# Performance work log

Hardware: AMD Instinct MI355X
Metric: run time of the kernel (lower is better)

## Reference

```python
import jax, jax.numpy as jnp
import numpy as np

VOCAB, HIDDEN, EMB_DIM = 30522, 768, 128
B, QLEN, DLEN = 1024, 32, 180
NEG = -1e4  # masked doc-token similarity
EPS = 1e-12


def setup_inputs() -> dict:
    key = jax.random.key(0)
    k1, k2, k3, k4, k5, k6 = jax.random.split(key, 6)
    return {
        "query_input_ids": jax.random.randint(k1, (B, QLEN), 0, VOCAB, dtype=jnp.int64) if jax.config.jax_enable_x64 else jax.random.randint(k1, (B, QLEN), 0, VOCAB, dtype=jnp.int32),
        "query_attention_mask": jax.random.randint(k2, (B, QLEN), 0, 2, dtype=jnp.int32),
        "doc_input_ids": jax.random.randint(k3, (B, DLEN), 0, VOCAB, dtype=jnp.int32),
        "doc_attention_mask": jax.random.randint(k4, (B, DLEN), 0, 2, dtype=jnp.int32),
        "embed_table": jax.random.normal(k5, (VOCAB, HIDDEN), dtype=jnp.float32) * 0.02,
        "proj_w": jax.random.normal(k6, (HIDDEN, EMB_DIM), dtype=jnp.float32) * 0.02,
        "proj_b": jnp.zeros((EMB_DIM,), dtype=jnp.float32),
    }


def _encode(ids, embed_table, proj_w, proj_b):
    # token embedding lookup -> linear projection -> L2 normalize (ColBERT-style)
    h = embed_table[ids]                      # (B, L, HIDDEN)
    e = jnp.einsum('blh,hd->bld', h, proj_w) + proj_b  # (B, L, EMB_DIM)
    e = e / (jnp.linalg.norm(e, axis=-1, keepdims=True) + EPS)
    return e


def reference(query_input_ids, query_attention_mask, doc_input_ids,
              doc_attention_mask, embed_table, proj_w, proj_b):
    q = _encode(query_input_ids, embed_table, proj_w, proj_b)  # (B, Q, D)
    d = _encode(doc_input_ids, embed_table, proj_w, proj_b)    # (B, T, D)
    # Batched MaxSim: sim[b,q,t] = <q_emb, d_emb>
    sim = jnp.einsum('bqd,btd->bqt', q, d)
    sim = jnp.where(doc_attention_mask[:, None, :] > 0, sim, NEG)
    max_sim = sim.max(axis=-1)                                  # (B, Q)
    scores = (max_sim * query_attention_mask.astype(max_sim.dtype)).sum(axis=-1)
    return scores  # (B,)
```

## Files before the change

kernel.cpp:

```cpp
#include <hip/hip_runtime.h>
#include <math.h>

#define VOCAB  30522
#define HIDDEN 768
#define EMB    128
#define BATCH  1024
#define QLEN   32
#define DLEN   180
#define NEGV   (-1e4f)

typedef __attribute__((ext_vector_type(8))) short bf16x8;
typedef __attribute__((ext_vector_type(4))) float f32x4;
typedef unsigned int u32;

__device__ __forceinline__ unsigned short f2bf(float x) {
  union { float f; unsigned u; } v; v.f = x;
  unsigned r = v.u + 0x7FFFu + ((v.u >> 16) & 1u);
  return (unsigned short)(r >> 16);
}
__device__ __forceinline__ float bf2f(unsigned short h) {
  union { float f; unsigned u; } v; v.u = ((unsigned)h) << 16;
  return v.f;
}
__device__ __forceinline__ void split_pk(float x0, float x1, unsigned& h, unsigned& l) {
  asm("v_cvt_pk_bf16_f32 %0, %1, %2" : "=v"(h) : "v"(x0), "v"(x1));
  float h0, h1;
  h0 = __uint_as_float(h << 16);
  h1 = __uint_as_float(h & 0xffff0000u);
  float l0 = x0 - h0, l1 = x1 - h1;
  asm("v_cvt_pk_bf16_f32 %0, %1, %2" : "=v"(l) : "v"(l0), "v"(l1));
}
__device__ __forceinline__ void gload16(const float* g, void* l) {
  __builtin_amdgcn_global_load_lds(
      (const __attribute__((address_space(1))) u32*)g,
      (__attribute__((address_space(3))) u32*)l, 16, 0, 0);
}

__global__ __launch_bounds__(256) void prep_wfrag(
    const float* __restrict__ W, unsigned short* __restrict__ wfh,
    unsigned short* __restrict__ wfl) {
  int g = blockIdx.x * 256 + threadIdx.x;
  if (g >= 24 * 8 * 64) return;
  int lane = g & 63, nt = (g >> 6) & 7, kk = g >> 9;
  int lr = lane & 15, kq = lane >> 4;
  int n = nt * 16 + lr;
  int k0 = kk * 32 + kq * 8;
  unsigned short hh[8], ll[8];
#pragma unroll
  for (int j = 0; j < 8; ++j) {
    float x = W[(size_t)(k0 + j) * EMB + n];
    unsigned short hi = f2bf(x);
    hh[j] = hi;
    ll[j] = f2bf(x - bf2f(hi));
  }
  size_t base = (size_t)g * 8;
#pragma unroll
  for (int j = 0; j < 2; ++j) {
    *(ushort4*)(wfh + base + j * 4) = *(ushort4*)(hh + j * 4);
    *(ushort4*)(wfl + base + j * 4) = *(ushort4*)(ll + j * 4);
  }
}

__global__ __launch_bounds__(256) void colbert_proj_mfma(
    const float* __restrict__ emb, const unsigned short* __restrict__ wfh,
    const unsigned short* __restrict__ wfl, const float* __restrict__ bias,
    unsigned short* __restrict__ pebf) {
  __shared__ __align__(16) char smem[17408];

  const int tid  = threadIdx.x;
  const int lane = tid & 63;
  const int wid  = tid >> 6;
  const int lr   = lane & 15;
  const int kq   = lane >> 4;
  const int row0 = blockIdx.x * 32;

#define GSRC(P, HC)                                                            \
  (emb + (size_t)(row0 + ((P) >> 4) > VOCAB - 1 ? VOCAB - 1                    \
                                                : row0 + ((P) >> 4)) * HIDDEN  \
       + (HC) * 64 + (((P) & 15) ^ (((P) >> 4) & 7)) * 4)

#define GLOAD(HC, BUF)                                                         \
  {                                                                            \
    char* d = smem + (BUF) * 8192;                                             \
    gload16(GSRC(tid, HC),       d + tid * 16);                                \
    gload16(GSRC(tid + 256, HC), d + 4096 + tid * 16);                         \
  }

  f32x4 acc[2][2];
#pragma unroll
  for (int mi = 0; mi < 2; ++mi)
#pragma unroll
    for (int ni = 0; ni < 2; ++ni) acc[mi][ni] = (f32x4)0.f;

  GLOAD(0, 0);
  __syncthreads();

  for (int hc = 0; hc < 12; ++hc) {
    const int cur = hc & 1;
    if (hc < 11) GLOAD(hc + 1, cur ^ 1);
    bf16x8 bh[2][2], bl[2][2];
#pragma unroll
    for (int kk = 0; kk < 2; ++kk)
#pragma unroll
      for (int ni = 0; ni < 2; ++ni) {
        size_t g = ((size_t)((hc * 2 + kk) * 8 + wid * 2 + ni) * 64 + lane) * 8;
        bh[kk][ni] = *(const bf16x8*)(wfh + g);
        bl[kk][ni] = *(const bf16x8*)(wfl + g);
      }
    char* Ab = smem + cur * 8192;
#pragma unroll
    for (int kk = 0; kk < 2; ++kk) {
      bf16x8 ah[2], al[2];
#pragma unroll
      for (int mi = 0; mi < 2; ++mi) {
        int row = mi * 16 + lr;
        int base = row * 256 + kk * 128 + kq * 32;
        float4 x0 = *(float4*)(Ab + ((base)      ^ ((row & 7) << 4)));
        float4 x1 = *(float4*)(Ab + ((base + 16) ^ ((row & 7) << 4)));
        union { unsigned u[4]; bf16x8 v; } H, L;
        split_pk(x0.x, x0.y, H.u[0], L.u[0]);
        split_pk(x0.z, x0.w, H.u[1], L.u[1]);
        split_pk(x1.x, x1.y, H.u[2], L.u[2]);
        split_pk(x1.z, x1.w, H.u[3], L.u[3]);
        ah[mi] = H.v; al[mi] = L.v;
      }
#pragma unroll
      for (int mi = 0; mi < 2; ++mi)
#pragma unroll
        for (int ni = 0; ni < 2; ++ni) {
          acc[mi][ni] = __builtin_amdgcn_mfma_f32_16x16x32_bf16(ah[mi], bh[kk][ni], acc[mi][ni], 0, 0, 0);
          acc[mi][ni] = __builtin_amdgcn_mfma_f32_16x16x32_bf16(ah[mi], bl[kk][ni], acc[mi][ni], 0, 0, 0);
          acc[mi][ni] = __builtin_amdgcn_mfma_f32_16x16x32_bf16(al[mi], bh[kk][ni], acc[mi][ni], 0, 0, 0);
        }
    }
    __syncthreads();
  }

  float* ep = (float*)smem;
#pragma unroll
  for (int ni = 0; ni < 2; ++ni) {
    int col = wid * 32 + ni * 16 + lr;
    float bb = bias[col];
#pragma unroll
    for (int mi = 0; mi < 2; ++mi)
#pragma unroll
      for (int j = 0; j < 4; ++j) {
        int r = mi * 16 + kq * 4 + j;
        ep[r * 132 + col] = acc[mi][ni][j] + bb;
      }
  }
  __syncthreads();
  {
    int row = tid >> 3, oct = tid & 7;
    float4 vv[4];
    float ss = 0.f;
#pragma unroll
    for (int i = 0; i < 4; ++i) {
      vv[i] = *(float4*)&ep[row * 132 + oct * 16 + i * 4];
      ss += vv[i].x * vv[i].x + vv[i].y * vv[i].y + vv[i].z * vv[i].z + vv[i].w * vv[i].w;
    }
    ss += __shfl_xor(ss, 1);
    ss += __shfl_xor(ss, 2);
    ss += __shfl_xor(ss, 4);
    float sc = 1.f / (sqrtf(ss) + 1e-12f);
    int gr = row0 + row;
    if (gr < VOCAB) {
      unsigned pk[8];
#pragma unroll
      for (int i = 0; i < 4; ++i) {
        pk[i * 2 + 0] = (unsigned)f2bf(vv[i].x * sc) | ((unsigned)f2bf(vv[i].y * sc) << 16);
        pk[i * 2 + 1] = (unsigned)f2bf(vv[i].z * sc) | ((unsigned)f2bf(vv[i].w * sc) << 16);
      }
      uint4* dst = (uint4*)(pebf + (size_t)gr * EMB + oct * 16);
      dst[0] = make_uint4(pk[0], pk[1], pk[2], pk[3]);
      dst[1] = make_uint4(pk[4], pk[5], pk[6], pk[7]);
    }
  }
#undef GSRC
#undef GLOAD
}

__global__ __launch_bounds__(256) void colbert_score_mfma(
    const int* __restrict__ qids, const int* __restrict__ qmask,
    const int* __restrict__ dids, const int* __restrict__ dmask,
    const unsigned short* __restrict__ pebf, float* __restrict__ out) {
  __shared__ int sqid[32];
  __shared__ int sdid[192];
  __shared__ unsigned char smsk[192];
  __shared__ float wmax[4][32];

  const int b    = blockIdx.x;
  const int tid  = threadIdx.x;
  const int lane = tid & 63;
  const int wid  = tid >> 6;
  const int lr   = lane & 15;
  const int kq   = lane >> 4;

  if (tid < 32) sqid[tid] = qids[b * QLEN + tid];
  if (tid < 192) {
    if (tid < DLEN) {
      sdid[tid] = dids[b * DLEN + tid];
      smsk[tid] = (unsigned char)(dmask[b * DLEN + tid] > 0 ? 1 : 0);
    } else {
      sdid[tid] = 0;
      smsk[tid] = 0;
    }
  }
  __syncthreads();

  bf16x8 af[2][4];
#pragma unroll
  for (int mi = 0; mi < 2; ++mi) {
    size_t base = (size_t)sqid[mi * 16 + lr] * EMB + kq * 8;
#pragma unroll
    for (int ks = 0; ks < 4; ++ks)
      af[mi][ks] = *(const bf16x8*)(pebf + base + ks * 32);
  }
  const int n0 = wid * 48;
  bf16x8 bfr[3][4];
#pragma unroll
  for (int ni = 0; ni < 3; ++ni) {
    size_t base = (size_t)sdid[n0 + ni * 16 + lr] * EMB + kq * 8;
#pragma unroll
    for (int ks = 0; ks < 4; ++ks)
      bfr[ni][ks] = *(const bf16x8*)(pebf + base + ks * 32);
  }

  f32x4 acc[2][3];
#pragma unroll
  for (int mi = 0; mi < 2; ++mi)
#pragma unroll
    for (int ni = 0; ni < 3; ++ni) acc[mi][ni] = (f32x4)0.f;

#pragma unroll
  for (int ks = 0; ks < 4; ++ks)
#pragma unroll
    for (int mi = 0; mi < 2; ++mi)
#pragma unroll
      for (int ni = 0; ni < 3; ++ni)
        acc[mi][ni] = __builtin_amdgcn_mfma_f32_16x16x32_bf16(af[mi][ks], bfr[ni][ks], acc[mi][ni], 0, 0, 0);

#pragma unroll
  for (int mi = 0; mi < 2; ++mi) {
#pragma unroll
    for (int j = 0; j < 4; ++j) {
      float m = -3.0e38f;
#pragma unroll
      for (int ni = 0; ni < 3; ++ni) {
        int t = n0 + ni * 16 + lr;
        float s = smsk[t] ? acc[mi][ni][j] : NEGV;
        m = fmaxf(m, s);
      }
#pragma unroll
      for (int x = 1; x < 16; x <<= 1) m = fmaxf(m, __shfl_xor(m, x));
      if (lr == 0) wmax[wid][mi * 16 + kq * 4 + j] = m;
    }
  }
  __syncthreads();

  if (tid < 32) {
    float m = fmaxf(fmaxf(wmax[0][tid], wmax[1][tid]),
                    fmaxf(wmax[2][tid], wmax[3][tid]));
    float s = m * (float)qmask[b * QLEN + tid];
#pragma unroll
    for (int x = 1; x < 32; x <<= 1) s += __shfl_xor(s, x);
    if (tid == 0) out[b] = s;
  }
}

extern "C" void kernel_launch(void* const* d_in, const int* in_sizes, int n_in,
                              void* d_out, int out_size, void* d_ws, size_t ws_size,
                              hipStream_t stream) {
  const int*   qids  = (const int*)d_in[0];
  const int*   qmask = (const int*)d_in[1];
  const int*   dids  = (const int*)d_in[2];
  const int*   dmask = (const int*)d_in[3];
  const float* emb   = (const float*)d_in[4];
  const float* W     = (const float*)d_in[5];
  const float* bias  = (const float*)d_in[6];
  float*       out   = (float*)d_out;

  char* ws = (char*)d_ws;
  unsigned short* pebf = (unsigned short*)ws;
  unsigned short* wfh  = (unsigned short*)(ws + 7813632);
  unsigned short* wfl  = (unsigned short*)(ws + 7813632 + 196608);

  prep_wfrag<<<48, 256, 0, stream>>>(W, wfh, wfl);
  colbert_proj_mfma<<<(VOCAB + 31) / 32, 256, 0, stream>>>(emb, wfh, wfl, bias, pebf);
  colbert_score_mfma<<<BATCH, 256, 0, stream>>>(qids, qmask, dids, dmask, pebf, out);
}
```

Before: 51.94 us.

## Shrink projection tile to 16 rows and preload full row slab into LDS

The vocabulary projection kernel now processes 16 embedding rows per block instead of 32, which doubles the grid size to raise parallelism across CUs. It replaces the double-buffered 64-column chunk pipeline with one upfront load of the whole 16x768 fp32 slab into 48KB of LDS, removing the per-iteration barriers. The trade-off is that each block re-reads the W fragments for half as many rows, doubling total W traffic, and the larger LDS footprint may limit how many blocks fit on a CU.

```diff
diff --git a/kernel.cpp b/kernel.cpp
--- a/kernel.cpp
+++ b/kernel.cpp
@@ -65,39 +65,31 @@
     const float* __restrict__ emb, const unsigned short* __restrict__ wfh,
     const unsigned short* __restrict__ wfl, const float* __restrict__ bias,
     unsigned short* __restrict__ pebf) {
-  __shared__ __align__(16) char smem[17408];
+  __shared__ __align__(16) char smem[49152];
 
   const int tid  = threadIdx.x;
   const int lane = tid & 63;
   const int wid  = tid >> 6;
   const int lr   = lane & 15;
   const int kq   = lane >> 4;
-  const int row0 = blockIdx.x * 32;
-
-#define GSRC(P, HC)                                                            \
-  (emb + (size_t)(row0 + ((P) >> 4) > VOCAB - 1 ? VOCAB - 1                    \
-                                                : row0 + ((P) >> 4)) * HIDDEN  \
-       + (HC) * 64 + (((P) & 15) ^ (((P) >> 4) & 7)) * 4)
-
-#define GLOAD(HC, BUF)                                                         \
-  {                                                                            \
-    char* d = smem + (BUF) * 8192;                                             \
-    gload16(GSRC(tid, HC),       d + tid * 16);                                \
-    gload16(GSRC(tid + 256, HC), d + 4096 + tid * 16);                         \
-  }
-
-  f32x4 acc[2][2];
-#pragma unroll
-  for (int mi = 0; mi < 2; ++mi)
-#pragma unroll
-    for (int ni = 0; ni < 2; ++ni) acc[mi][ni] = (f32x4)0.f;
-
-  GLOAD(0, 0);
-  __syncthreads();
+  const int row0 = blockIdx.x * 16;
+
+  {
+    int srow = tid >> 4;
+    int gr = row0 + srow; if (gr > VOCAB - 1) gr = VOCAB - 1;
+    const float* rowp = emb + (size_t)gr * HIDDEN
+                        + (size_t)(((tid & 15) ^ (srow & 7)) * 4);
+#pragma unroll
+    for (int i = 0; i < 12; ++i) {
+      gload16(rowp + i * 64, smem + i * 4096 + tid * 16);
+    }
+  }
+  __syncthreads();
+
+  f32x4 acc[2];
+  acc[0] = (f32x4)0.f; acc[1] = (f32x4)0.f;
 
   for (int hc = 0; hc < 12; ++hc) {
-    const int cur = hc & 1;
-    if (hc < 11) GLOAD(hc + 1, cur ^ 1);
     bf16x8 bh[2][2], bl[2][2];
 #pragma unroll
     for (int kk = 0; kk < 2; ++kk)
@@ -107,77 +99,59 @@
         bh[kk][ni] = *(const bf16x8*)(wfh + g);
         bl[kk][ni] = *(const bf16x8*)(wfl + g);
       }
-    char* Ab = smem + cur * 8192;
+    char* Ab = smem + hc * 4096;
 #pragma unroll
     for (int kk = 0; kk < 2; ++kk) {
-      bf16x8 ah[2], al[2];
-#pragma unroll
-      for (int mi = 0; mi < 2; ++mi) {
-        int row = mi * 16 + lr;
-        int base = row * 256 + kk * 128 + kq * 32;
-        float4 x0 = *(float4*)(Ab + ((base)      ^ ((row & 7) << 4)));
-        float4 x1 = *(float4*)(Ab + ((base + 16) ^ ((row & 7) << 4)));
-        union { unsigned u[4]; bf16x8 v; } H, L;
-        split_pk(x0.x, x0.y, H.u[0], L.u[0]);
-        split_pk(x0.z, x0.w, H.u[1], L.u[1]);
-        split_pk(x1.x, x1.y, H.u[2], L.u[2]);
-        split_pk(x1.z, x1.w, H.u[3], L.u[3]);
-        ah[mi] = H.v; al[mi] = L.v;
+      int s0 = kk * 8 + kq * 2;
+      float4 x0 = *(float4*)(Ab + lr * 256 + ((s0)     ^ (lr & 7)) * 16);
+      float4 x1 = *(float4*)(Ab + lr * 256 + ((s0 + 1) ^ (lr & 7)) * 16);
+      union { unsigned u[4]; bf16x8 v; } H, L;
+      split_pk(x0.x, x0.y, H.u[0], L.u[0]);
+      split_pk(x0.z, x0.w, H.u[1], L.u[1]);
+      split_pk(x1.x, x1.y, H.u[2], L.u[2]);
+      split_pk(x1.z, x1.w, H.u[3], L.u[3]);
+#pragma unroll
+      for (int ni = 0; ni < 2; ++ni) {
+        acc[ni] = __builtin_amdgcn_mfma_f32_16x16x32_bf16(H.v, bh[kk][ni], acc[ni], 0, 0, 0);
+        acc[ni] = __builtin_amdgcn_mfma_f32_16x16x32_bf16(H.v, bl[kk][ni], acc[ni], 0, 0, 0);
+        acc[ni] = __builtin_amdgcn_mfma_f32_16x16x32_bf16(L.v, bh[kk][ni], acc[ni], 0, 0, 0);
       }
-#pragma unroll
-      for (int mi = 0; mi < 2; ++mi)
-#pragma unroll
-        for (int ni = 0; ni < 2; ++ni) {
-          acc[mi][ni] = __builtin_amdgcn_mfma_f32_16x16x32_bf16(ah[mi], bh[kk][ni], acc[mi][ni], 0, 0, 0);
-          acc[mi][ni] = __builtin_amdgcn_mfma_f32_16x16x32_bf16(ah[mi], bl[kk][ni], acc[mi][ni], 0, 0, 0);
-          acc[mi][ni] = __builtin_amdgcn_mfma_f32_16x16x32_bf16(al[mi], bh[kk][ni], acc[mi][ni], 0, 0, 0);
-        }
-    }
-    __syncthreads();
-  }
-
+    }
+  }
+
+  __syncthreads();
   float* ep = (float*)smem;
 #pragma unroll
   for (int ni = 0; ni < 2; ++ni) {
     int col = wid * 32 + ni * 16 + lr;
     float bb = bias[col];
 #pragma unroll
-    for (int mi = 0; mi < 2; ++mi)
-#pragma unroll
-      for (int j = 0; j < 4; ++j) {
-        int r = mi * 16 + kq * 4 + j;
-        ep[r * 132 + col] = acc[mi][ni][j] + bb;
-      }
+    for (int j = 0; j < 4; ++j) {
+      int r = kq * 4 + j;
+      ep[r * 132 + col] = acc[ni][j] + bb;
+    }
   }
   __syncthreads();
   {
-    int row = tid >> 3, oct = tid & 7;
-    float4 vv[4];
-    float ss = 0.f;
-#pragma unroll
-    for (int i = 0; i < 4; ++i) {
-      vv[i] = *(float4*)&ep[row * 132 + oct * 16 + i * 4];
-      ss += vv[i].x * vv[i].x + vv[i].y * vv[i].y + vv[i].z * vv[i].z + vv[i].w * vv[i].w;
-    }
+    int row = tid >> 4, g = tid & 15;
+    float4 v0 = *(float4*)&ep[row * 132 + g * 8];
+    float4 v1 = *(float4*)&ep[row * 132 + g * 8 + 4];
+    float ss = v0.x * v0.x + v0.y * v0.y + v0.z * v0.z + v0.w * v0.w
+             + v1.x * v1.x + v1.y * v1.y + v1.z * v1.z + v1.w * v1.w;
     ss += __shfl_xor(ss, 1);
     ss += __shfl_xor(ss, 2);
     ss += __shfl_xor(ss, 4);
+    ss += __shfl_xor(ss, 8);
     float sc = 1.f / (sqrtf(ss) + 1e-12f);
     int gr = row0 + row;
     if (gr < VOCAB) {
-      unsigned pk[8];
-#pragma unroll
-      for (int i = 0; i < 4; ++i) {
-        pk[i * 2 + 0] = (unsigned)f2bf(vv[i].x * sc) | ((unsigned)f2bf(vv[i].y * sc) << 16);
-        pk[i * 2 + 1] = (unsigned)f2bf(vv[i].z * sc) | ((unsigned)f2bf(vv[i].w * sc) << 16);
-      }
-      uint4* dst = (uint4*)(pebf + (size_t)gr * EMB + oct * 16);
-      dst[0] = make_uint4(pk[0], pk[1], pk[2], pk[3]);
-      dst[1] = make_uint4(pk[4], pk[5], pk[6], pk[7]);
-    }
-  }
-#undef GSRC
-#undef GLOAD
+      unsigned pk0 = (unsigned)f2bf(v0.x * sc) | ((unsigned)f2bf(v0.y * sc) << 16);
+      unsigned pk1 = (unsigned)f2bf(v0.z * sc) | ((unsigned)f2bf(v0.w * sc) << 16);
+      unsigned pk2 = (unsigned)f2bf(v1.x * sc) | ((unsigned)f2bf(v1.y * sc) << 16);
+      unsigned pk3 = (unsigned)f2bf(v1.z * sc) | ((unsigned)f2bf(v1.w * sc) << 16);
+      *(uint4*)(pebf + (size_t)gr * EMB + g * 8) = make_uint4(pk0, pk1, pk2, pk3);
+    }
+  }
 }
 
 __global__ __launch_bounds__(256) void colbert_score_mfma(
@@ -286,6 +260,6 @@
   unsigned short* wfl  = (unsigned short*)(ws + 7813632 + 196608);
 
   prep_wfrag<<<48, 256, 0, stream>>>(W, wfh, wfl);
-  colbert_proj_mfma<<<(VOCAB + 31) / 32, 256, 0, stream>>>(emb, wfh, wfl, bias, pebf);
+  colbert_proj_mfma<<<(VOCAB + 15) / 16, 256, 0, stream>>>(emb, wfh, wfl, bias, pebf);
   colbert_score_mfma<<<BATCH, 256, 0, stream>>>(qids, qmask, dids, dmask, pebf, out);
 }
```

Measured after the change: 63.41 us. 1.22x slower.
